# Performance work log

Measured on AMD Instinct MI355X. Metric: run time of the kernel, lower is better.

The kernel has to match this reference:

```python
import jax, jax.numpy as jnp
import numpy as np

N_E = 8192
E_DIM = 64
BETA = 0.25
DIVERSITY_GAMMA = 1.0
INV_TEMP = 100.0
EPS = 1e-05


def _entropy(p):
    # matches torch: (-p * log(clamp(p, min=eps))).sum(-1)
    return (-p * jnp.log(jnp.clip(p, EPS))).sum(axis=-1)


def setup_inputs() -> dict:
    key = jax.random.key(0)
    k1, k2 = jax.random.split(key)
    z = jax.random.normal(k1, (16, E_DIM, 32, 32), dtype=jnp.float32)
    # codebook, init like nn.Embedding then uniform_(-1/n_e, 1/n_e) scale doesn't matter for math;
    # use a small uniform init faithful to the module
    emb = jax.random.uniform(k2, (N_E, E_DIM), dtype=jnp.float32,
                             minval=-1.0 / N_E, maxval=1.0 / N_E)
    return {"z": z, "emb": emb}


def reference(z, emb):
    sg = jax.lax.stop_gradient
    # b c h w -> b h w c
    zp = jnp.transpose(z, (0, 2, 3, 1))            # [B,H,W,C]
    zf = zp.reshape(-1, E_DIM)                      # [N, C]
    # pairwise squared distances: ||z||^2 + ||e||^2 - 2 z e^T
    d = (jnp.sum(zf * zf, axis=1, keepdims=True)
         + jnp.sum(emb * emb, axis=1)
         - 2.0 * jnp.einsum('nd,kd->nk', zf, emb))  # [N, n_e]
    min_indices = jnp.argmin(d, axis=1)             # [N]
    z_q = emb[min_indices].reshape(zp.shape)        # gather, [B,H,W,C]
    # legacy commitment loss
    loss = (jnp.mean((sg(z_q) - zp) ** 2)
            + BETA * jnp.mean((z_q - sg(zp)) ** 2))
    # entropy aux loss (frac_per_sample_entropy == 1.0)
    prob = jax.nn.softmax(-d * INV_TEMP, axis=-1)   # [N, n_e]
    per_sample_entropy = _entropy(prob).mean()
    avg_prob = prob.mean(axis=0)                    # [n_e]
    codebook_entropy = _entropy(avg_prob)
    entropy_aux = per_sample_entropy - DIVERSITY_GAMMA * codebook_entropy
    # straight-through estimator
    z_q = zp + sg(z_q - zp)
    quantized = jnp.transpose(z_q, (0, 3, 1, 2))    # b h w c -> b c h w
    return quantized, loss, entropy_aux, min_indices
```

## Files before the change

kernel.cpp:

```cpp
#include <hip/hip_runtime.h>
#include <cfloat>


typedef __attribute__((ext_vector_type(8))) short short8v;
typedef __attribute__((ext_vector_type(4))) float f32x4;

#define C100L2E 144.26950408889634f
#define C200L2E 288.53900817779268f
#define LN2 0.6931471805599453

#define BLOB_TILE 33792
#define OFF_BLOB   0
#define OFF_INVZ   2162688
#define OFF_MINIDX 2228224
#define OFF_AVG    2293760
#define OFF_PSE    2326528
#define OFF_ZPART  2326544
#define OFF_S1PART (OFF_ZPART + 262144)
#define OFF_DMPART (OFF_S1PART + 262144)
#define OFF_IMPART (OFF_DMPART + 262144)
#define OFF_LOSSP  (OFF_IMPART + 262144)

__device__ __forceinline__ unsigned short f2bf_rne(float f) {
    unsigned u = __float_as_uint(f);
    u = (u + 0x7fffu + ((u >> 16) & 1u)) >> 16;
    return (unsigned short)u;
}

__device__ __forceinline__ void gload_lds16(const void* g, void* l) {
    __builtin_amdgcn_global_load_lds(
        (const __attribute__((address_space(1))) unsigned int*)g,
        (__attribute__((address_space(3))) unsigned int*)l, 16, 0, 0);
}

__global__ __launch_bounds__(256) void k_prep(const float* __restrict__ emb,
                                              char* __restrict__ blob) {
    const int k = blockIdx.x * 256 + threadIdx.x;
    const float* row = emb + k * 64;
    float fv[64];
#pragma unroll
    for (int i = 0; i < 16; ++i) {
        float4 v = ((const float4*)row)[i];
        fv[4 * i] = v.x; fv[4 * i + 1] = v.y; fv[4 * i + 2] = v.z; fv[4 * i + 3] = v.w;
    }
    float r8[8];
#pragma unroll
    for (int j = 0; j < 8; ++j) r8[j] = __fmul_rn(fv[j], fv[j]);
#pragma unroll
    for (int i = 8; i < 64; i += 8)
#pragma unroll
        for (int j = 0; j < 8; ++j)
            r8[j] = __fadd_rn(r8[j], __fmul_rn(fv[i + j], fv[i + j]));
    float s01 = __fadd_rn(r8[0], r8[1]), s23 = __fadd_rn(r8[2], r8[3]);
    float s45 = __fadd_rn(r8[4], r8[5]), s67 = __fadd_rn(r8[6], r8[7]);
    float e2 = __fadd_rn(__fadd_rn(s01, s23), __fadd_rn(s45, s67));

    char* tb = blob + (size_t)(k >> 7) * BLOB_TILE;
    const int r = k & 127;
    ((float*)(tb + 32768))[r] = e2;
    const int sw = (r & 7) << 4;
#pragma unroll
    for (int dh = 0; dh < 2; ++dh)
#pragma unroll
        for (int cg = 0; cg < 4; ++cg) {
            short8v hv, lv;
#pragma unroll
            for (int e = 0; e < 8; ++e) {
                float f = fv[dh * 32 + cg * 8 + e];
                unsigned short hb = f2bf_rne(f);
                float hf = __uint_as_float((unsigned)hb << 16);
                hv[e] = (short)hb;
                lv[e] = (short)f2bf_rne(f - hf);
            }
            const int byt = (r * 128 + dh * 64 + cg * 16) ^ sw;
            *(short8v*)(tb + byt) = hv;
            *(short8v*)(tb + 16384 + byt) = lv;
        }
}

#define STAGE_EMB(DSTBASE, TILE)                                                  \
    {                                                                             \
        const char* gsrc = blob + (size_t)(TILE) * BLOB_TILE;                     \
        char* ldst = (DSTBASE) + ((tid >> 6) << 10);                              \
        const char* g = gsrc + tid * 16;                                          \
        _Pragma("unroll")                                                         \
        for (int q = 0; q < 8; ++q)                                               \
            gload_lds16(g + q * 4096, ldst + q * 4096);                           \
        if (tid < 32) gload_lds16(gsrc + 32768 + tid * 16, (DSTBASE) + 32768);    \
    }

__global__ __launch_bounds__(256) void k_pass1(
    const float* __restrict__ z, const char* __restrict__ blob,
    float* __restrict__ Zpart, float* __restrict__ S1part,
    float* __restrict__ dmpart, int* __restrict__ impart)
{
    __shared__ __align__(16) char smem[BLOB_TILE];
    __shared__ float zzsh[64];
    float (*zt)[68] = (float (*)[68])smem;

    const int tid = threadIdx.x;
    const int panel = blockIdx.x >> 2;
    const int ks = blockIdx.x & 3;
    const int n0 = panel * 64;

    {
        const int c = tid & 63, rq = (tid >> 6) * 16;
        const float* src = z + ((n0 >> 10) * 64 + c) * 1024 + (n0 & 1023) + rq;
#pragma unroll
        for (int i = 0; i < 4; ++i) {
            float4 v = ((const float4*)src)[i];
            *(float4*)&zt[c][rq + 4 * i] = v;
        }
    }
    __syncthreads();
    if (tid < 64) {
        float r8[8];
#pragma unroll
        for (int j = 0; j < 8; ++j) { float v = zt[j][tid]; r8[j] = __fmul_rn(v, v); }
#pragma unroll
        for (int i = 8; i < 64; i += 8)
#pragma unroll
            for (int j = 0; j < 8; ++j) {
                float v = zt[i + j][tid];
                r8[j] = __fadd_rn(r8[j], __fmul_rn(v, v));
            }
        float s01 = __fadd_rn(r8[0], r8[1]), s23 = __fadd_rn(r8[2], r8[3]);
        float s45 = __fadd_rn(r8[4], r8[5]), s67 = __fadd_rn(r8[6], r8[7]);
        zzsh[tid] = __fadd_rn(__fadd_rn(s01, s23), __fadd_rn(s45, s67));
    }

    const int ln = tid & 63, wv = tid >> 6;
    const int lr = ln & 15, lg = ln >> 4;

    short8v Ah[2], Al[2];
#pragma unroll
    for (int s = 0; s < 2; ++s) {
        const int row = wv * 16 + lr;
        const int db = s * 32 + lg * 8;
#pragma unroll
        for (int j = 0; j < 8; ++j) {
            float f = zt[db + j][row];
            unsigned short hb = f2bf_rne(f);
            float hf = __uint_as_float((unsigned)hb << 16);
            Ah[s][j] = (short)hb;
            Al[s][j] = (short)f2bf_rne(f - hf);
        }
    }
    __syncthreads();

    float zzr[4];
#pragma unroll
    for (int rg = 0; rg < 4; ++rg) zzr[rg] = zzsh[wv * 16 + lg * 4 + rg];

    STAGE_EMB(smem, ks * 16);

    float Zp[4] = {0.f, 0.f, 0.f, 0.f}, S1p[4] = {0.f, 0.f, 0.f, 0.f};
    float dmin[4] = {FLT_MAX, FLT_MAX, FLT_MAX, FLT_MAX};
    int imin[4] = {0, 0, 0, 0};

    for (int it = 0; it < 16; ++it) {
        const int kbase = ks * 2048 + it * 128;
        __syncthreads();

        f32x4 acc[8];
#pragma unroll
        for (int f = 0; f < 8; ++f) { f32x4 zv = {0.f, 0.f, 0.f, 0.f}; acc[f] = zv; }

#pragma unroll
        for (int f = 0; f < 8; ++f) {
            const int rr = f * 16 + lr;
            const int sw2 = (rr & 7) << 4;
            short8v Bh[2], Bl[2];
#pragma unroll
            for (int s = 0; s < 2; ++s) {
                const int byt = (rr * 128 + s * 64 + lg * 16) ^ sw2;
                Bh[s] = *(const short8v*)(smem + byt);
                Bl[s] = *(const short8v*)(smem + 16384 + byt);
            }
#pragma unroll
            for (int s = 0; s < 2; ++s) {
                acc[f] = __builtin_amdgcn_mfma_f32_16x16x32_bf16(Ah[s], Bh[s], acc[f], 0, 0, 0);
                acc[f] = __builtin_amdgcn_mfma_f32_16x16x32_bf16(Ah[s], Bl[s], acc[f], 0, 0, 0);
                acc[f] = __builtin_amdgcn_mfma_f32_16x16x32_bf16(Al[s], Bh[s], acc[f], 0, 0, 0);
                acc[f] = __builtin_amdgcn_mfma_f32_16x16x32_bf16(Al[s], Bl[s], acc[f], 0, 0, 0);
            }
        }

        float e2v[8];
#pragma unroll
        for (int f = 0; f < 8; ++f)
            e2v[f] = *(const float*)(smem + 32768 + (f * 16 + lr) * 4);

        __syncthreads();
        if (it < 15) STAGE_EMB(smem, ks * 16 + it + 1);

#pragma unroll
        for (int f = 0; f < 8; ++f) {
            const float c2 = e2v[f] * C100L2E;
            const int kk = kbase + f * 16 + lr;
#pragma unroll
            for (int rg = 0; rg < 4; ++rg) {
                const float sdot = acc[f][rg];
                const float t = fmaf(sdot, C200L2E, -c2);
                const float ex = __builtin_amdgcn_exp2f(t);
                Zp[rg] += ex;
                S1p[rg] = fmaf(t, ex, S1p[rg]);
                const float dnp = __fsub_rn(__fadd_rn(zzr[rg], e2v[f]),
                                            __fmul_rn(2.f, sdot));
                if (dnp < dmin[rg]) { dmin[rg] = dnp; imin[rg] = kk; }
            }
        }
    }

#pragma unroll
    for (int msk = 1; msk < 16; msk <<= 1) {
#pragma unroll
        for (int rg = 0; rg < 4; ++rg) {
            float d2 = __shfl_xor(dmin[rg], msk, 16);
            int i2 = __shfl_xor(imin[rg], msk, 16);
            float Z2 = __shfl_xor(Zp[rg], msk, 16);
            float s2 = __shfl_xor(S1p[rg], msk, 16);
            if (d2 < dmin[rg] || (d2 == dmin[rg] && i2 < imin[rg])) {
                dmin[rg] = d2; imin[rg] = i2;
            }
            Zp[rg] += Z2;
            S1p[rg] += s2;
        }
    }
    if (lr == 0) {
#pragma unroll
        for (int rg = 0; rg < 4; ++rg) {
            const int n = n0 + wv * 16 + lg * 4 + rg;
            Zpart[ks * 16384 + n] = Zp[rg];
            S1part[ks * 16384 + n] = S1p[rg];
            dmpart[ks * 16384 + n] = dmin[rg];
            impart[ks * 16384 + n] = imin[rg];
        }
    }
}

__global__ __launch_bounds__(256) void k_rowred(
    const float* __restrict__ Zpart, const float* __restrict__ S1part,
    const float* __restrict__ dmpart, const int* __restrict__ impart,
    float* __restrict__ invZ, int* __restrict__ minidx,
    float* __restrict__ out_idx, double* __restrict__ pse_sum)
{
    const int n = blockIdx.x * 256 + threadIdx.x;
    float Z = __fadd_rn(__fadd_rn(Zpart[n], Zpart[16384 + n]),
                        __fadd_rn(Zpart[32768 + n], Zpart[49152 + n]));
    float S1 = __fadd_rn(__fadd_rn(S1part[n], S1part[16384 + n]),
                         __fadd_rn(S1part[32768 + n], S1part[49152 + n]));
    float dm = dmpart[n];
    int im = impart[n];
#pragma unroll
    for (int ksp = 1; ksp < 4; ++ksp) {
        float d2 = dmpart[ksp * 16384 + n];
        int i2 = impart[ksp * 16384 + n];
        if (d2 < dm || (d2 == dm && i2 < im)) { dm = d2; im = i2; }
    }
    minidx[n] = im;
    out_idx[n] = (float)im;
    float iz = 1.0f / Z;
    invZ[n] = iz;
    double h = log((double)Z) - LN2 * (double)S1 * (double)iz;
#pragma unroll
    for (int m = 32; m > 0; m >>= 1) h += __shfl_xor(h, m, 64);
    if ((threadIdx.x & 63) == 0) atomicAdd(pse_sum, h);
}

__global__ __launch_bounds__(256) void k_pass2(
    const float* __restrict__ z, const char* __restrict__ blob,
    const float* __restrict__ invZ, float* __restrict__ avg_acc)
{
    __shared__ __align__(16) char smem[51456];
    char* regB = smem + 33792;
    float* izC = (float*)(smem + 51200);

    const int tid = threadIdx.x;
    const int kt = blockIdx.x & 63;
    const int ns = blockIdx.x >> 6;
    const int ln = tid & 63, wv = tid >> 6;
    const int lr = ln & 15, lg = ln >> 4;

    const char* zsrc[5]; char* zdst[5]; bool zok[5];
#pragma unroll
    for (int q = 0; q < 5; ++q) {
        const int off_w = q * 1024 + ln * 16;
        const int c_local = off_w / 272;
        const int rem = off_w - c_local * 272;
        zok[q] = (off_w < 4352) && (rem < 256);
        const int r4f = rem >> 2;
        zsrc[q] = (const char*)(z + (ns * 64 + wv * 16 + c_local) * 1024 + r4f);
        zdst[q] = regB + wv * 4352 + q * 1024;
    }

    STAGE_EMB(smem, kt);
#pragma unroll
    for (int q = 0; q < 5; ++q)
        if (zok[q]) gload_lds16(zsrc[q], zdst[q]);
    if (tid < 16)
        gload_lds16((const char*)(invZ + ns * 1024) + tid * 16, izC);
    __syncthreads();

    float e2v[8];
#pragma unroll
    for (int f = 0; f < 8; ++f)
        e2v[f] = *(const float*)(smem + 32768 + (f * 16 + lr) * 4);

    float acck[8] = {0.f, 0.f, 0.f, 0.f, 0.f, 0.f, 0.f, 0.f};

    for (int it = 0; it < 16; ++it) {
        short8v Ah[2], Al[2];
#pragma unroll
        for (int s = 0; s < 2; ++s) {
            const int row = wv * 16 + lr;
            const int db = s * 32 + lg * 8;
#pragma unroll
            for (int j = 0; j < 8; ++j) {
                float f = *(const float*)(regB + (db + j) * 272 + row * 4);
                unsigned short hb = f2bf_rne(f);
                float hf = __uint_as_float((unsigned)hb << 16);
                Ah[s][j] = (short)hb;
                Al[s][j] = (short)f2bf_rne(f - hf);
            }
        }
        float izr[4];
#pragma unroll
        for (int rg = 0; rg < 4; ++rg) izr[rg] = izC[wv * 16 + lg * 4 + rg];

        f32x4 acc[8];
#pragma unroll
        for (int f = 0; f < 8; ++f) { f32x4 zv = {0.f, 0.f, 0.f, 0.f}; acc[f] = zv; }

#pragma unroll
        for (int f = 0; f < 8; ++f) {
            const int rr = f * 16 + lr;
            const int sw2 = (rr & 7) << 4;
            short8v Bh[2], Bl[2];
#pragma unroll
            for (int s = 0; s < 2; ++s) {
                const int byt = (rr * 128 + s * 64 + lg * 16) ^ sw2;
                Bh[s] = *(const short8v*)(smem + byt);
                Bl[s] = *(const short8v*)(smem + 16384 + byt);
            }
#pragma unroll
            for (int s = 0; s < 2; ++s) {
                acc[f] = __builtin_amdgcn_mfma_f32_16x16x32_bf16(Ah[s], Bh[s], acc[f], 0, 0, 0);
                acc[f] = __builtin_amdgcn_mfma_f32_16x16x32_bf16(Ah[s], Bl[s], acc[f], 0, 0, 0);
                acc[f] = __builtin_amdgcn_mfma_f32_16x16x32_bf16(Al[s], Bh[s], acc[f], 0, 0, 0);
                acc[f] = __builtin_amdgcn_mfma_f32_16x16x32_bf16(Al[s], Bl[s], acc[f], 0, 0, 0);
            }
        }

        __syncthreads();
        if (it < 15) {
#pragma unroll
            for (int q = 0; q < 5; ++q)
                if (zok[q]) gload_lds16(zsrc[q] + (it + 1) * 256, zdst[q]);
            if (tid < 16)
                gload_lds16((const char*)(invZ + ns * 1024 + (it + 1) * 64) + tid * 16, izC);
        }

#pragma unroll
        for (int f = 0; f < 8; ++f) {
            const float c2 = e2v[f] * C100L2E;
#pragma unroll
            for (int rg = 0; rg < 4; ++rg) {
                const float t = fmaf(acc[f][rg], C200L2E, -c2);
                const float ex = __builtin_amdgcn_exp2f(t);
                acck[f] = fmaf(ex, izr[rg], acck[f]);
            }
        }
        __syncthreads();
    }

#pragma unroll
    for (int f = 0; f < 8; ++f) {
        float cs = acck[f];
        cs += __shfl_xor(cs, 16, 64);
        cs += __shfl_xor(cs, 32, 64);
        if (lg == 0) atomicAdd(&avg_acc[kt * 128 + f * 16 + lr], cs);
    }
}

__global__ __launch_bounds__(256) void k_quant(
    const float* __restrict__ z, const float* __restrict__ emb,
    const int* __restrict__ minidx, float* __restrict__ out,
    double* __restrict__ loss_part)
{
    __shared__ float lred[4];
    const int o = blockIdx.x * 256 + threadIdx.x;
    const int n = ((o >> 16) << 10) + (o & 1023);
    const int c = (o >> 10) & 63;
    const int idx = minidx[n];
    const float e = emb[idx * 64 + c];
    const float zv = z[o];
    out[o] = e;
    float d = e - zv;
    float sq = d * d;
#pragma unroll
    for (int m = 32; m > 0; m >>= 1) sq += __shfl_xor(sq, m, 64);
    if ((threadIdx.x & 63) == 0) lred[threadIdx.x >> 6] = sq;
    __syncthreads();
    if (threadIdx.x == 0)
        loss_part[blockIdx.x] = (double)lred[0] + (double)lred[1]
                              + (double)lred[2] + (double)lred[3];
}

__global__ __launch_bounds__(256) void k_final(
    const float* __restrict__ avg_acc, const double* __restrict__ pse_sum,
    const double* __restrict__ loss_part, float* __restrict__ out)
{
    __shared__ double red[256];
    const int tid = threadIdx.x;

    double lsum = 0.0;
    for (int k = tid; k < 4096; k += 256) lsum += loss_part[k];
    red[tid] = lsum;
    __syncthreads();
    for (int s = 128; s > 0; s >>= 1) {
        if (tid < s) red[tid] += red[tid + s];
        __syncthreads();
    }
    double ltot = red[0];
    __syncthreads();

    double local = 0.0;
    for (int k = tid; k < 8192; k += 256) {
        float p = avg_acc[k] * (1.0f / 16384.0f);
        float cl = fmaxf(p, 1e-5f);
        local += (double)(-p * logf(cl));
    }
    red[tid] = local;
    __syncthreads();
    for (int s = 128; s > 0; s >>= 1) {
        if (tid < s) red[tid] += red[tid + s];
        __syncthreads();
    }
    if (tid == 0) {
        double ce = red[0];
        double pse = pse_sum[0] / 16384.0;
        out[1048576] = (float)(1.25 * ltot / 1048576.0);
        out[1048577] = (float)(pse - ce);
    }
}

extern "C" void kernel_launch(void* const* d_in, const int* in_sizes, int n_in,
                              void* d_out, int out_size, void* d_ws, size_t ws_size,
                              hipStream_t stream) {
    const float* z = (const float*)d_in[0];
    const float* emb = (const float*)d_in[1];
    float* out = (float*)d_out;
    char* ws = (char*)d_ws;
    char* blob = ws + OFF_BLOB;
    float* invZ = (float*)(ws + OFF_INVZ);
    int* minidx = (int*)(ws + OFF_MINIDX);
    float* avg_acc = (float*)(ws + OFF_AVG);
    double* pse_sum = (double*)(ws + OFF_PSE);
    float* Zpart = (float*)(ws + OFF_ZPART);
    float* S1part = (float*)(ws + OFF_S1PART);
    float* dmpart = (float*)(ws + OFF_DMPART);
    int* impart = (int*)(ws + OFF_IMPART);
    double* loss_part = (double*)(ws + OFF_LOSSP);

    hipMemsetAsync(ws + OFF_AVG, 0, 32768 + 16, stream);

    k_prep<<<32, 256, 0, stream>>>(emb, blob);
    k_pass1<<<1024, 256, 0, stream>>>(z, blob, Zpart, S1part, dmpart, impart);
    k_rowred<<<64, 256, 0, stream>>>(Zpart, S1part, dmpart, impart,
                                     invZ, minidx, out + 1048578, pse_sum);
    k_pass2<<<1024, 256, 0, stream>>>(z, blob, invZ, avg_acc);
    k_quant<<<4096, 256, 0, stream>>>(z, emb, minidx, out, loss_part);
    k_final<<<1, 256, 0, stream>>>(avg_acc, pse_sum, loss_part, out);
}
```

Baseline: 198.7 us.

## Cache pre-split bf16 z panels from pass1 and use 2x M-tiling in pass2

Pass1 now writes the hi/lo bf16 split of each z panel into scratch space inside the output buffer. Pass2 reads these pre-split fragments straight from global memory, so it no longer transposes z through LDS or redoes the conversion. Each wave now covers two 16-row M tiles per iteration, which reuses the codebook B fragments across more MFMAs and halves the iteration count. The per-iteration barriers are dropped and all invZ values are loaded up front. This relies on the output buffer being safe to use as scratch until k_quant overwrites it, and it raises register pressure.

```diff
diff --git a/kernel.cpp b/kernel.cpp
--- a/kernel.cpp
+++ b/kernel.cpp
@@ -91,6 +91,7 @@
 
 __global__ __launch_bounds__(256) void k_pass1(
     const float* __restrict__ z, const char* __restrict__ blob,
+    char* __restrict__ zblob,
     float* __restrict__ Zpart, float* __restrict__ S1part,
     float* __restrict__ dmpart, int* __restrict__ impart)
 {
@@ -144,6 +145,17 @@
             float hf = __uint_as_float((unsigned)hb << 16);
             Ah[s][j] = (short)hb;
             Al[s][j] = (short)f2bf_rne(f - hf);
+        }
+    }
+
+    if (ks == 0) {
+        char* tb = zblob + (size_t)panel * 16384;
+        const int rowp = wv * 16 + lr;
+#pragma unroll
+        for (int s = 0; s < 2; ++s) {
+            const int byt = rowp * 128 + s * 64 + lg * 16;
+            *(short8v*)(tb + byt) = Ah[s];
+            *(short8v*)(tb + 8192 + byt) = Al[s];
         }
     }
     __syncthreads();
@@ -269,12 +281,11 @@
 }
 
 __global__ __launch_bounds__(256) void k_pass2(
-    const float* __restrict__ z, const char* __restrict__ blob,
+    const char* __restrict__ zblob, const char* __restrict__ blob,
     const float* __restrict__ invZ, float* __restrict__ avg_acc)
 {
-    __shared__ __align__(16) char smem[51456];
-    char* regB = smem + 33792;
-    float* izC = (float*)(smem + 51200);
+    __shared__ __align__(16) char smem[BLOB_TILE + 4096];
+    float* izAll = (float*)(smem + BLOB_TILE);
 
     const int tid = threadIdx.x;
     const int kt = blockIdx.x & 63;
@@ -282,24 +293,9 @@
     const int ln = tid & 63, wv = tid >> 6;
     const int lr = ln & 15, lg = ln >> 4;
 
-    const char* zsrc[5]; char* zdst[5]; bool zok[5];
-#pragma unroll
-    for (int q = 0; q < 5; ++q) {
-        const int off_w = q * 1024 + ln * 16;
-        const int c_local = off_w / 272;
-        const int rem = off_w - c_local * 272;
-        zok[q] = (off_w < 4352) && (rem < 256);
-        const int r4f = rem >> 2;
-        zsrc[q] = (const char*)(z + (ns * 64 + wv * 16 + c_local) * 1024 + r4f);
-        zdst[q] = regB + wv * 4352 + q * 1024;
-    }
-
     STAGE_EMB(smem, kt);
-#pragma unroll
-    for (int q = 0; q < 5; ++q)
-        if (zok[q]) gload_lds16(zsrc[q], zdst[q]);
-    if (tid < 16)
-        gload_lds16((const char*)(invZ + ns * 1024) + tid * 16, izC);
+    gload_lds16((const char*)(invZ + ns * 1024) + tid * 16,
+                (char*)izAll + (wv << 10));
     __syncthreads();
 
     float e2v[8];
@@ -309,28 +305,34 @@
 
     float acck[8] = {0.f, 0.f, 0.f, 0.f, 0.f, 0.f, 0.f, 0.f};
 
-    for (int it = 0; it < 16; ++it) {
-        short8v Ah[2], Al[2];
-#pragma unroll
-        for (int s = 0; s < 2; ++s) {
-            const int row = wv * 16 + lr;
-            const int db = s * 32 + lg * 8;
-#pragma unroll
-            for (int j = 0; j < 8; ++j) {
-                float f = *(const float*)(regB + (db + j) * 272 + row * 4);
-                unsigned short hb = f2bf_rne(f);
-                float hf = __uint_as_float((unsigned)hb << 16);
-                Ah[s][j] = (short)hb;
-                Al[s][j] = (short)f2bf_rne(f - hf);
-            }
-        }
-        float izr[4];
-#pragma unroll
-        for (int rg = 0; rg < 4; ++rg) izr[rg] = izC[wv * 16 + lg * 4 + rg];
-
-        f32x4 acc[8];
-#pragma unroll
-        for (int f = 0; f < 8; ++f) { f32x4 zv = {0.f, 0.f, 0.f, 0.f}; acc[f] = zv; }
+    for (int it = 0; it < 8; ++it) {
+        short8v Ah[2][2], Al[2][2];
+        const int p64 = ns * 16 + it * 2 + (wv >> 1);
+        const char* tb = zblob + (size_t)p64 * 16384;
+#pragma unroll
+        for (int m = 0; m < 2; ++m) {
+            const int rowp = (wv & 1) * 32 + m * 16 + lr;
+#pragma unroll
+            for (int s = 0; s < 2; ++s) {
+                const int byt = rowp * 128 + s * 64 + lg * 16;
+                Ah[m][s] = *(const short8v*)(tb + byt);
+                Al[m][s] = *(const short8v*)(tb + 8192 + byt);
+            }
+        }
+        const int izb = it * 128 + wv * 32 + lg * 4;
+        float4 iz0 = *(const float4*)&izAll[izb];
+        float4 iz1 = *(const float4*)&izAll[izb + 16];
+        float izr[2][4] = {{iz0.x, iz0.y, iz0.z, iz0.w},
+                           {iz1.x, iz1.y, iz1.z, iz1.w}};
+
+        f32x4 acc[2][8];
+#pragma unroll
+        for (int m = 0; m < 2; ++m)
+#pragma unroll
+            for (int f = 0; f < 8; ++f) {
+                f32x4 zv = {0.f, 0.f, 0.f, 0.f};
+                acc[m][f] = zv;
+            }
 
 #pragma unroll
         for (int f = 0; f < 8; ++f) {
@@ -344,34 +346,28 @@
                 Bl[s] = *(const short8v*)(smem + 16384 + byt);
             }
 #pragma unroll
-            for (int s = 0; s < 2; ++s) {
-                acc[f] = __builtin_amdgcn_mfma_f32_16x16x32_bf16(Ah[s], Bh[s], acc[f], 0, 0, 0);
-                acc[f] = __builtin_amdgcn_mfma_f32_16x16x32_bf16(Ah[s], Bl[s], acc[f], 0, 0, 0);
-                acc[f] = __builtin_amdgcn_mfma_f32_16x16x32_bf16(Al[s], Bh[s], acc[f], 0, 0, 0);
-                acc[f] = __builtin_amdgcn_mfma_f32_16x16x32_bf16(Al[s], Bl[s], acc[f], 0, 0, 0);
-            }
-        }
-
-        __syncthreads();
-        if (it < 15) {
-#pragma unroll
-            for (int q = 0; q < 5; ++q)
-                if (zok[q]) gload_lds16(zsrc[q] + (it + 1) * 256, zdst[q]);
-            if (tid < 16)
-                gload_lds16((const char*)(invZ + ns * 1024 + (it + 1) * 64) + tid * 16, izC);
+            for (int s = 0; s < 2; ++s)
+#pragma unroll
+                for (int m = 0; m < 2; ++m) {
+                    acc[m][f] = __builtin_amdgcn_mfma_f32_16x16x32_bf16(Ah[m][s], Bh[s], acc[m][f], 0, 0, 0);
+                    acc[m][f] = __builtin_amdgcn_mfma_f32_16x16x32_bf16(Ah[m][s], Bl[s], acc[m][f], 0, 0, 0);
+                    acc[m][f] = __builtin_amdgcn_mfma_f32_16x16x32_bf16(Al[m][s], Bh[s], acc[m][f], 0, 0, 0);
+                    acc[m][f] = __builtin_amdgcn_mfma_f32_16x16x32_bf16(Al[m][s], Bl[s], acc[m][f], 0, 0, 0);
+                }
         }
 
 #pragma unroll
         for (int f = 0; f < 8; ++f) {
             const float c2 = e2v[f] * C100L2E;
 #pragma unroll
-            for (int rg = 0; rg < 4; ++rg) {
-                const float t = fmaf(acc[f][rg], C200L2E, -c2);
-                const float ex = __builtin_amdgcn_exp2f(t);
-                acck[f] = fmaf(ex, izr[rg], acck[f]);
-            }
-        }
-        __syncthreads();
+            for (int m = 0; m < 2; ++m)
+#pragma unroll
+                for (int rg = 0; rg < 4; ++rg) {
+                    const float t = fmaf(acc[m][f][rg], C200L2E, -c2);
+                    const float ex = __builtin_amdgcn_exp2f(t);
+                    acck[f] = fmaf(ex, izr[m][rg], acck[f]);
+                }
+        }
     }
 
 #pragma unroll
@@ -462,14 +458,15 @@
     float* dmpart = (float*)(ws + OFF_DMPART);
     int* impart = (int*)(ws + OFF_IMPART);
     double* loss_part = (double*)(ws + OFF_LOSSP);
+    char* zblob = (char*)d_out;
 
     hipMemsetAsync(ws + OFF_AVG, 0, 32768 + 16, stream);
 
     k_prep<<<32, 256, 0, stream>>>(emb, blob);
-    k_pass1<<<1024, 256, 0, stream>>>(z, blob, Zpart, S1part, dmpart, impart);
+    k_pass1<<<1024, 256, 0, stream>>>(z, blob, zblob, Zpart, S1part, dmpart, impart);
     k_rowred<<<64, 256, 0, stream>>>(Zpart, S1part, dmpart, impart,
                                      invZ, minidx, out + 1048578, pse_sum);
-    k_pass2<<<1024, 256, 0, stream>>>(z, blob, invZ, avg_acc);
+    k_pass2<<<1024, 256, 0, stream>>>(zblob, blob, invZ, avg_acc);
     k_quant<<<4096, 256, 0, stream>>>(z, emb, minidx, out, loss_part);
     k_final<<<1, 256, 0, stream>>>(avg_acc, pse_sum, loss_part, out);
 }
```

New measurement: 187.5 us. 5.6% less time.
